# Performance work log

Hardware: AMD Instinct MI355X
Metric: run time of the kernel (lower is better)

## Reference

```python
import jax, jax.numpy as jnp
import numpy as np

B, T, N, H = 16, 12, 1000, 128
NL = 2  # num_layers
EPS = 1e-5


def setup_inputs() -> dict:
    key = jax.random.key(0)
    ks = jax.random.split(key, 16)
    rn = lambda k, s, sc=0.05: jax.random.normal(k, s, jnp.float32) * sc
    return {
        "inputs": jax.random.normal(ks[0], (B, T, N), jnp.float32),
        "adj": jax.random.uniform(ks[1], (N, N), dtype=jnp.float32),
        # per-layer graph-conv params (stacked over NL layers)
        "gc1_w": rn(ks[2], (NL, H + 1, 2 * H)),
        "gc1_b": jnp.ones((NL, 2 * H), jnp.float32),   # bias=1.0 in torch init
        "gc2_w": rn(ks[3], (NL, H + 1, H)),
        "gc2_b": jnp.zeros((NL, H), jnp.float32),
        "ln_g": jnp.ones((NL, H), jnp.float32),
        "ln_b": jnp.zeros((NL, H), jnp.float32),
        "res_w": rn(ks[4], (H,)),   # Linear(1,H) weight squeezed
        "res_b": rn(ks[5], (H,)),
        # GRU tail (unidirectional, 1 layer)
        "gru_wih": rn(ks[6], (3 * H, H)),
        "gru_whh": rn(ks[7], (3 * H, H)),
        "gru_bih": rn(ks[8], (3 * H,)),
        "gru_bhh": rn(ks[9], (3 * H,)),
        "proj_w": rn(ks[10], (H, H)),
        "proj_b": rn(ks[11], (H,)),
        # output MLP
        "out_w1": rn(ks[12], (256, H)),
        "out_b1": rn(ks[13], (256,)),
        "out_w2": rn(ks[14], (H, 256)),
        "out_b2": rn(ks[15], (H,)),
    }


def _laplacian(adj):
    a = jax.nn.softmax(adj, axis=-1)
    m = a + jnp.eye(N, dtype=adj.dtype)           # A + I
    d = m.sum(axis=1)
    dis = jnp.where(d > 0, d ** -0.5, 0.0)
    # matrix.matmul(D^-1/2).T.matmul(D^-1/2)
    return (m * dis[None, :]).T * dis[None, :]


def _gconv(L, x, h, w, b):
    # x: [B,N], h: [B,N,H], concat: [B,N,H+1]
    concat = jnp.concatenate([x[..., None], h], axis=2)
    ac = jnp.einsum("mn,bnk->bmk", L, concat)     # Laplacian graph conv
    return ac @ w + b                              # [B,N,out_dim]


def _cell(L, x, h, w1, b1, w2, b2):
    gates = jax.nn.sigmoid(_gconv(L, x, h, w1, b1))       # [B,N,2H]
    # torch chunks the FLAT [B, N*2H] tensor: split is across nodes!
    flat = gates.reshape(gates.shape[0], N * 2 * H)
    r = flat[:, : N * H].reshape(-1, N, H)
    u = flat[:, N * H :].reshape(-1, N, H)
    c = jnp.tanh(_gconv(L, x, r * h, w2, b2))
    return u * h + (1.0 - u) * c


def _layernorm(x, g, b):
    mu = x.mean(-1, keepdims=True)
    var = jnp.mean((x - mu) ** 2, axis=-1, keepdims=True)
    return (x - mu) * jax.lax.rsqrt(var + EPS) * g + b


def _gru_last(xs, h0, wih, whh, bih, bhh):
    # xs: [T, BN, H]
    def step(h, x):
        gi = x @ wih.T + bih
        gh = h @ whh.T + bhh
        ir, iz, inn = jnp.split(gi, 3, axis=-1)
        hr, hz, hn = jnp.split(gh, 3, axis=-1)
        r = jax.nn.sigmoid(ir + hr)
        z = jax.nn.sigmoid(iz + hz)
        n = jnp.tanh(inn + r * hn)
        return (1.0 - z) * n + z * h, None
    h_last, _ = jax.lax.scan(step, h0, xs)
    return h_last


def reference(inputs, adj, gc1_w, gc1_b, gc2_w, gc2_b, ln_g, ln_b, res_w, res_b,
              gru_wih, gru_whh, gru_bih, gru_bhh, proj_w, proj_b,
              out_w1, out_b1, out_w2, out_b2):
    L = _laplacian(adj)

    def step(hs, x_t):
        x = x_t
        residual = x_t
        new_hs = []
        out = None
        for i in range(NL):
            h = _cell(L, x, hs[i], gc1_w[i], gc1_b[i], gc2_w[i], gc2_b[i])
            new_hs.append(h)
            res = residual[..., None] * res_w + res_b   # Linear(1,H)
            out = _layernorm(h + res, ln_g[i], ln_b[i])  # dropout = identity (eval)
            x = out.mean(axis=2)
            residual = x
        return tuple(new_hs), out

    h0 = tuple(jnp.zeros((B, N, H), jnp.float32) for _ in range(NL))
    xs = jnp.swapaxes(inputs, 0, 1)                 # [T,B,N]
    _, outs = jax.lax.scan(step, h0, xs)            # [T,B,N,H]

    # GRU tail over time, batched across B*N node-sequences
    rnn_xs = jnp.transpose(outs, (0, 1, 2, 3)).reshape(T, B * N, H)
    h_last = _gru_last(rnn_xs, jnp.zeros((B * N, H), jnp.float32),
                       gru_wih, gru_whh, gru_bih, gru_bhh)
    last = h_last @ proj_w.T + proj_b
    o = last.reshape(B, N, H)
    o = jax.nn.relu(o @ out_w1.T + out_b1) @ out_w2.T + out_b2
    return o
```

## Files before the change

### kernel.cpp

```cpp
#include <hip/hip_runtime.h>
#include <math.h>

#define BB 16
#define TT 12
#define NN 1000
#define HH 128
#define CC 129
#define NROW 16000
#define GR 160
#define KP 1024
#define CP2 160
#define SPS 168

#define BUFSZ 26624
#define OFF_SP   79872
#define OFF_SCAL 101376
#define OFF_SST  103936
#define SMEMB    108032
#define OFF_SO   20480

typedef __attribute__((ext_vector_type(4))) float f32x4;
typedef __attribute__((ext_vector_type(8))) __bf16 bf16x8;

#define MFMA16(A, B, C) __builtin_amdgcn_mfma_f32_16x16x32_bf16((A), (B), (C), 0, 0, 0)

__device__ __forceinline__ float sigmoidf_(float x) { return 1.0f / (1.0f + expf(-x)); }

__global__ void k_softmax(const float* __restrict__ adj, float* __restrict__ a) {
    int i = blockIdx.x;
    int t = threadIdx.x;
    __shared__ float red[256];
    float m = -1e30f;
    for (int j = t; j < NN; j += 256) m = fmaxf(m, adj[i * NN + j]);
    red[t] = m; __syncthreads();
    for (int s = 128; s > 0; s >>= 1) { if (t < s) red[t] = fmaxf(red[t], red[t + s]); __syncthreads(); }
    m = red[0]; __syncthreads();
    float sum = 0.f;
    for (int j = t; j < NN; j += 256) sum += expf(adj[i * NN + j] - m);
    red[t] = sum; __syncthreads();
    for (int s = 128; s > 0; s >>= 1) { if (t < s) red[t] += red[t + s]; __syncthreads(); }
    float inv = 1.0f / red[0];
    for (int j = t; j < NN; j += 256) a[i * NN + j] = expf(adj[i * NN + j] - m) * inv;
}

__global__ __launch_bounds__(256) void k_build_Lt(const float* __restrict__ a, __bf16* __restrict__ Lb) {
    __shared__ float s[64][65];
    int bi = blockIdx.x * 64;
    int bj = blockIdx.y * 64;
    int t = threadIdx.x;
    for (int q = t; q < 64 * 64; q += 256) {
        int r = q >> 6, c = q & 63;
        int jj = bj + r, ii = bi + c;
        s[r][c] = (jj < NN && ii < NN) ? a[jj * NN + ii] : 0.f;
    }
    __syncthreads();
    for (int q = t; q < 64 * 64; q += 256) {
        int r = q >> 6, c = q & 63;
        int ii = bi + r, jj = bj + c;
        if (ii < NN && jj < NN)
            Lb[(size_t)ii * KP + jj] = (__bf16)(0.5f * (s[c][r] + (ii == jj ? 1.0f : 0.0f)));
    }
}

__global__ void k_prep(const float* __restrict__ wih, const float* __restrict__ whh,
                       const float* __restrict__ proj_w, const float* __restrict__ ow1,
                       const float* __restrict__ ow2, const float* __restrict__ gc1_w,
                       const float* __restrict__ gc2_w,
                       __bf16* __restrict__ WihB, __bf16* __restrict__ WhhB,
                       __bf16* __restrict__ projB, __bf16* __restrict__ w1B,
                       __bf16* __restrict__ w2B, __bf16* __restrict__ W1t,
                       __bf16* __restrict__ W2t) {
    int idx = blockIdx.x * 256 + threadIdx.x;
    if (idx < 49152) { WihB[idx] = (__bf16)wih[idx]; return; }
    idx -= 49152;
    if (idx < 49152) { WhhB[idx] = (__bf16)whh[idx]; return; }
    idx -= 49152;
    if (idx < 16384) { projB[idx] = (__bf16)proj_w[idx]; return; }
    idx -= 16384;
    if (idx < 32768) { w1B[idx] = (__bf16)ow1[idx]; return; }
    idx -= 32768;
    if (idx < 32768) { w2B[idx] = (__bf16)ow2[idx]; return; }
    idx -= 32768;
    if (idx < 2 * 256 * CP2) {
        int l = idx / (256 * CP2); int r = idx % (256 * CP2); int o = r / CP2, c = r % CP2;
        W1t[idx] = (c < CC) ? (__bf16)gc1_w[((size_t)l * CC + c) * 256 + o] : (__bf16)0.f;
        return;
    }
    idx -= 2 * 256 * CP2;
    if (idx < 2 * 128 * CP2) {
        int l = idx / (128 * CP2); int r = idx % (128 * CP2); int o = r / CP2, c = r % CP2;
        W2t[idx] = (c < CC) ? (__bf16)gc2_w[((size_t)l * CC + c) * 128 + o] : (__bf16)0.f;
    }
}

__global__ void k_prep_x(const float* __restrict__ inp, __bf16* __restrict__ G0) {
    int idx = blockIdx.x * 256 + threadIdx.x;
    if (idx >= BB * 1024) return;
    int b = idx >> 10, k = idx & 1023;
    G0[(size_t)b * GR * KP + k] = (k < NN) ? (__bf16)inp[(size_t)b * TT * NN + k] : (__bf16)0.f;
}

#define GL16(SRC, DSTOFF)                                                            \
    __builtin_amdgcn_global_load_lds(                                                \
        (const __attribute__((address_space(1))) unsigned int*)(SRC),                \
        (__attribute__((address_space(3))) unsigned int*)(smem + (DSTOFF)), 16, 0, 0)

template<int MODE, int STORE>
__global__ __launch_bounds__(1024) void k_fused(
    const __bf16* __restrict__ Lb, const __bf16* __restrict__ Gf,
    const __bf16* __restrict__ Wt, const float* __restrict__ bias,
    __bf16* __restrict__ GB, float* __restrict__ u, float* __restrict__ h,
    const float* __restrict__ x_in, int xstride,
    const float* __restrict__ res_w, const float* __restrict__ res_b,
    const float* __restrict__ ln_g, const float* __restrict__ ln_b,
    float* __restrict__ x_out, __bf16* __restrict__ Gnext,
    __bf16* __restrict__ GhSelf,
    float* __restrict__ hg, __bf16* __restrict__ Hb,
    const __bf16* __restrict__ WihB, const __bf16* __restrict__ WhhB,
    const float* __restrict__ bih, const float* __restrict__ bhh,
    const float* __restrict__ inp, __bf16* __restrict__ xnextG, int tnext)
{
    __shared__ __align__(16) char smem[SMEMB];
    __bf16* sP   = (__bf16*)(smem + OFF_SP);
    __bf16* sGT  = (__bf16*)smem;
    __bf16* sT   = (__bf16*)smem;
    __bf16* sO   = (__bf16*)(smem + OFF_SO);
    float*  sScal= (float*)(smem + OFF_SCAL);
    float*  sSt  = (float*)(smem + OFF_SST);

    int tid = threadIdx.x;
    int wg = blockIdx.x;
    int b = wg & 15;
    int m0 = (wg >> 4) * 64;
    int wave = tid >> 6, lane = tid & 63;
    int lr = lane & 15, lk = lane >> 4;
    int wm = wave >> 3;
    int wcg = wave & 7;
    int cgbase = (wcg == 0) ? 0 : (wcg + 1) * 16;
    int NC = (wcg == 0) ? 2 : 1;

    if (MODE == 0) {
        if (tid < 256) sScal[tid] = bias[tid];
    } else if (tid < 128) {
        sScal[tid] = bias[tid];
        sScal[128 + tid] = res_w[tid];
        sScal[256 + tid] = res_b[tid];
        sScal[384 + tid] = ln_g[tid];
        sScal[512 + tid] = ln_b[tid];
    }

    size_t srowOff = (size_t)b * GR * KP;
    int rIn = lane >> 3;
    int cswz = ((lane & 7) ^ rIn) * 8;

    int ch0 = (wave < 10) ? (2 * wave) : (wave + 10);
    int ch1 = 2 * wave + 1;
    const __bf16* src0 = (ch0 < 8)
        ? Lb + (size_t)(m0 + ch0 * 8 + rIn) * KP + cswz
        : Gf + srowOff + (size_t)((ch0 - 8) * 8 + rIn) * KP + cswz;
    const __bf16* src1 = (wave < 10)
        ? ((ch1 < 8) ? Lb + (size_t)(m0 + ch1 * 8 + rIn) * KP + cswz
                     : Gf + srowOff + (size_t)((ch1 - 8) * 8 + rIn) * KP + cswz)
        : (const __bf16*)nullptr;

#define STAGE(BUF, IT) {                                                \
    GL16(src0 + (IT) * 64, (BUF) * BUFSZ + ch0 * 1024);                 \
    if (wave < 10) GL16(src1 + (IT) * 64, (BUF) * BUFSZ + ch1 * 1024); }

    f32x4 acc[2][2];
#pragma unroll
    for (int i = 0; i < 2; i++)
#pragma unroll
        for (int j = 0; j < 2; j++) acc[i][j] = (f32x4){0.f, 0.f, 0.f, 0.f};

    STAGE(0, 0);
    STAGE(1, 1);
    int bc = 0;
    for (int it = 0; it < 16; ++it) {
        if (it == 15)       asm volatile("s_waitcnt vmcnt(0)" ::: "memory");
        else if (wave < 10) asm volatile("s_waitcnt vmcnt(2)" ::: "memory");
        else                asm volatile("s_waitcnt vmcnt(1)" ::: "memory");
        __builtin_amdgcn_s_barrier();
        __builtin_amdgcn_sched_barrier(0);
        const char* bp = smem + bc * BUFSZ;
#pragma unroll
        for (int ks = 0; ks < 2; ks++) {
            int kb = (ks * 64 + lk * 16) ^ ((lr & 7) << 4);
            bf16x8 af[2];
#pragma unroll
            for (int mf = 0; mf < 2; mf++) {
                int chA = wm * 4 + mf * 2 + (lr >> 3);
                af[mf] = *(const bf16x8*)(bp + chA * 1024 + (lr & 7) * 128 + kb);
            }
#pragma unroll
            for (int cf = 0; cf < 2; cf++) {
                if (cf < NC) {
                    int chB = 8 + (cgbase >> 3) + cf * 2 + (lr >> 3);
                    bf16x8 bfr = *(const bf16x8*)(bp + chB * 1024 + (lr & 7) * 128 + kb);
                    acc[0][cf] = MFMA16(af[0], bfr, acc[0][cf]);
                    acc[1][cf] = MFMA16(af[1], bfr, acc[1][cf]);
                }
            }
        }
        if (it < 14) { int bs = (it + 2) % 3; STAGE(bs, it + 2); }
        bc = (bc == 2) ? 0 : bc + 1;
    }
    __syncthreads();
#undef STAGE

#pragma unroll
    for (int mf = 0; mf < 2; mf++)
#pragma unroll
        for (int cf = 0; cf < 2; cf++) {
            if (cf < NC) {
#pragma unroll
                for (int i = 0; i < 4; i++)
                    sP[(wm * 32 + mf * 16 + lk * 4 + i) * SPS + cgbase + cf * 16 + lr] =
                        (__bf16)acc[mf][cf][i];
            }
        }
    for (int q = tid; q < 64 * 16; q += 1024) sP[(q >> 4) * SPS + 144 + (q & 15)] = (__bf16)0.f;
    __syncthreads();

    constexpr int NOF = (MODE == 0) ? 2 : 1;
    int o0 = wave * NOF * 16;
    f32x4 accs[4][NOF];
#pragma unroll
    for (int i = 0; i < 4; i++)
#pragma unroll
        for (int j = 0; j < NOF; j++) accs[i][j] = (f32x4){0.f, 0.f, 0.f, 0.f};
    if (wave < 8) {
#pragma unroll
        for (int kk2 = 0; kk2 < CP2; kk2 += 32) {
            bf16x8 pa[4];
#pragma unroll
            for (int mf2 = 0; mf2 < 4; mf2++)
                pa[mf2] = *(const bf16x8*)&sP[(mf2 * 16 + lr) * SPS + kk2 + lk * 8];
#pragma unroll
            for (int of = 0; of < NOF; of++) {
                bf16x8 wb = *(const bf16x8*)&Wt[(size_t)(o0 + of * 16 + lr) * CP2 + kk2 + lk * 8];
#pragma unroll
                for (int mf2 = 0; mf2 < 4; mf2++)
                    accs[mf2][of] = MFMA16(pa[mf2], wb, accs[mf2][of]);
            }
        }
    }

    if (MODE == 0) {
        if (tid < 8)
            *(bf16x8*)&GB[srowOff + m0 + tid * 8] = *(const bf16x8*)&Gf[srowOff + m0 + tid * 8];
        bool clean = (m0 + 64 <= 500);
        if (clean) {
            if (wave < 8) {
#pragma unroll
                for (int mf2 = 0; mf2 < 4; mf2++)
#pragma unroll
                    for (int of = 0; of < NOF; of++) {
                        int o = o0 + of * 16 + lr;
                        float bv = sScal[o];
#pragma unroll
                        for (int i = 0; i < 4; i++)
                            sGT[o * 72 + mf2 * 16 + lk * 4 + i] = (__bf16)sigmoidf_(accs[mf2][of][i] + bv);
                    }
            }
            __syncthreads();
            for (int q = tid; q < 128 * 16; q += 1024) {
                int j = q >> 4;
                int rnc = (q & 15) * 4;
                size_t gidx = srowOff + (size_t)(1 + j) * KP + 2 * m0 + rnc * 2;
                bf16x8 hv = *(const bf16x8*)&Gf[gidx];
                bf16x8 rv;
#pragma unroll
                for (int e = 0; e < 8; e++) {
                    int rnl = rnc + (e >> 1);
                    int hi = e & 1;
                    float g = (float)sGT[(hi * 128 + j) * 72 + rnl];
                    rv[e] = (__bf16)(g * (float)hv[e]);
                }
                *(bf16x8*)&GB[gidx] = rv;
            }
        } else if (wave < 8) {
#pragma unroll
            for (int mf2 = 0; mf2 < 4; mf2++)
#pragma unroll
                for (int of = 0; of < NOF; of++) {
                    int o = o0 + of * 16 + lr;
                    int j = o & 127, hi = o >> 7;
                    float bv = sScal[o];
#pragma unroll
                    for (int i = 0; i < 4; i++) {
                        int m = m0 + mf2 * 16 + lk * 4 + i;
                        if (m >= NN) continue;
                        float g = sigmoidf_(accs[mf2][of][i] + bv);
                        if (m < 500) {
                            size_t gi = srowOff + (size_t)(1 + j) * KP + 2 * m + hi;
                            GB[gi] = (__bf16)(g * (float)Gf[gi]);
                        } else {
                            u[((size_t)b * NN + 2 * (m - 500) + hi) * HH + j] = g;
                        }
                    }
                }
        }
    } else {
        int j = o0 + lr;
        float hnv[4][4];
        float mu_[4][4], rs_[4][4];
        float xs_[4][4];
        if (wave < 8) {
            float s_[4][4], ss_[4][4];
#pragma unroll
            for (int a = 0; a < 4; a++)
#pragma unroll
                for (int i = 0; i < 4; i++) { s_[a][i] = 0.f; ss_[a][i] = 0.f; }
            float b2v = sScal[j], rwv = sScal[128 + j], rbv = sScal[256 + j];
#pragma unroll
            for (int mf2 = 0; mf2 < 4; mf2++) {
#pragma unroll
                for (int i = 0; i < 4; i++) {
                    int m = m0 + mf2 * 16 + lk * 4 + i;
                    int msafe = (m < NN) ? m : (NN - 1);
                    size_t ri = ((size_t)b * NN + msafe) * HH + j;
                    float cv = tanhf(accs[mf2][0][i] + b2v);
                    float uu = u[ri];
                    float hv = h[ri];
                    float hn = uu * hv + (1.f - uu) * cv;
                    if (m < NN) h[ri] = hn;
                    hnv[mf2][i] = hn;
                    float xv = (m < NN) ? x_in[(size_t)b * xstride + m] : 0.f;
                    float y = hn + xv * rwv + rbv;
                    accs[mf2][0][i] = y;
                    s_[mf2][i] += y; ss_[mf2][i] += y * y;
                }
            }
#pragma unroll
            for (int msk = 1; msk < 16; msk <<= 1)
#pragma unroll
                for (int a = 0; a < 4; a++)
#pragma unroll
                    for (int i = 0; i < 4; i++) {
                        s_[a][i] += __shfl_xor(s_[a][i], msk);
                        ss_[a][i] += __shfl_xor(ss_[a][i], msk);
                    }
            if (lr == 0) {
#pragma unroll
                for (int a = 0; a < 4; a++)
#pragma unroll
                    for (int i = 0; i < 4; i++) {
                        int ml = a * 16 + lk * 4 + i;
                        sSt[wave * 64 + ml] = s_[a][i];
                        sSt[512 + wave * 64 + ml] = ss_[a][i];
                    }
            }
        }
        __syncthreads();
        if (wave < 8) {
#pragma unroll
            for (int a = 0; a < 4; a++)
#pragma unroll
                for (int i = 0; i < 4; i++) {
                    int ml = a * 16 + lk * 4 + i;
                    float S = 0.f, SS = 0.f;
#pragma unroll
                    for (int w = 0; w < 8; w++) { S += sSt[w * 64 + ml]; SS += sSt[512 + w * 64 + ml]; }
                    float mu = S * (1.f / 128.f);
                    float var = SS * (1.f / 128.f) - mu * mu;
                    mu_[a][i] = mu;
                    rs_[a][i] = rsqrtf(var + 1e-5f);
                }
            float lg = sScal[384 + j], lb2 = sScal[512 + j];
#pragma unroll
            for (int mf2 = 0; mf2 < 4; mf2++)
#pragma unroll
                for (int i = 0; i < 4; i++) {
                    float ov = (accs[mf2][0][i] - mu_[mf2][i]) * rs_[mf2][i] * lg + lb2;
                    accs[mf2][0][i] = ov;
                    xs_[mf2][i] = ov;
                }
#pragma unroll
            for (int msk = 1; msk < 16; msk <<= 1)
#pragma unroll
                for (int a = 0; a < 4; a++)
#pragma unroll
                    for (int i = 0; i < 4; i++) xs_[a][i] += __shfl_xor(xs_[a][i], msk);
        }
        __syncthreads();
        if (wave < 8 && lr == 0) {
#pragma unroll
            for (int a = 0; a < 4; a++)
#pragma unroll
                for (int i = 0; i < 4; i++)
                    sSt[wave * 64 + a * 16 + lk * 4 + i] = xs_[a][i];
        }
        __syncthreads();
        if (wave == 0 && lr == 0) {
#pragma unroll
            for (int a = 0; a < 4; a++)
#pragma unroll
                for (int i = 0; i < 4; i++) {
                    int ml = a * 16 + lk * 4 + i;
                    int m = m0 + ml;
                    if (m < NN) {
                        float S = 0.f;
#pragma unroll
                        for (int w = 0; w < 8; w++) S += sSt[w * 64 + ml];
                        float xv = S * (1.f / 128.f);
                        if (x_out) x_out[(size_t)b * NN + m] = xv;
                        if (Gnext) Gnext[(size_t)b * GR * KP + m] = (__bf16)xv;
                    }
                }
        }
        if (wave < 8) {
#pragma unroll
            for (int mf2 = 0; mf2 < 4; mf2++)
#pragma unroll
                for (int i = 0; i < 4; i++)
                    sT[j * 72 + mf2 * 16 + lk * 4 + i] = (__bf16)hnv[mf2][i];
            if (STORE) {
#pragma unroll
                for (int mf2 = 0; mf2 < 4; mf2++)
#pragma unroll
                    for (int i = 0; i < 4; i++)
                        sO[(mf2 * 16 + lk * 4 + i) * 136 + j] = (__bf16)accs[mf2][0][i];
            }
        }
        __syncthreads();
        for (int q = tid; q < 128 * 8; q += 1024) {
            int jj = q >> 3, mc = (q & 7) * 8;
            if (m0 + mc < NN)
                *(bf16x8*)&GhSelf[srowOff + (size_t)(1 + jj) * KP + m0 + mc] =
                    *(const bf16x8*)&sT[jj * 72 + mc];
        }
        if (STORE) {
            if (wave < 8) {
                float br  = bih[j] + bhh[j];
                float bz  = bih[128 + j] + bhh[128 + j];
                float bni = bih[256 + j], bnh = bhh[256 + j];
                const __bf16* wir = WihB + (size_t)j * HH;
                const __bf16* whr = WhhB + (size_t)j * HH;
                const __bf16* wiz = WihB + (size_t)(128 + j) * HH;
                const __bf16* whz = WhhB + (size_t)(128 + j) * HH;
                const __bf16* win = WihB + (size_t)(256 + j) * HH;
                const __bf16* whn = WhhB + (size_t)(256 + j) * HH;
#pragma unroll
                for (int mf = 0; mf < 4; mf++) {
                    f32x4 gr = (f32x4){0.f,0.f,0.f,0.f}, gz = gr, gni = gr, gnh = gr;
                    int rrow = m0 + mf * 16 + lr;
                    size_t hrow = (size_t)b * NN + ((rrow < NN) ? rrow : (NN - 1));
#pragma unroll
                    for (int kk = 0; kk < 128; kk += 32) {
                        bf16x8 xa = *(const bf16x8*)&sO[(mf * 16 + lr) * 136 + kk + lk * 8];
                        bf16x8 ha = *(const bf16x8*)&Hb[hrow * HH + kk + lk * 8];
                        gr  = MFMA16(xa, *(const bf16x8*)(wir + kk + lk * 8), gr);
                        gr  = MFMA16(ha, *(const bf16x8*)(whr + kk + lk * 8), gr);
                        gz  = MFMA16(xa, *(const bf16x8*)(wiz + kk + lk * 8), gz);
                        gz  = MFMA16(ha, *(const bf16x8*)(whz + kk + lk * 8), gz);
                        gni = MFMA16(xa, *(const bf16x8*)(win + kk + lk * 8), gni);
                        gnh = MFMA16(ha, *(const bf16x8*)(whn + kk + lk * 8), gnh);
                    }
#pragma unroll
                    for (int i = 0; i < 4; i++) {
                        int m = m0 + mf * 16 + lk * 4 + i;
                        if (m >= NN) continue;
                        size_t ri = ((size_t)b * NN + m) * HH + j;
                        float hv = hg[ri];
                        float rg = sigmoidf_(gr[i] + br);
                        float zg = sigmoidf_(gz[i] + bz);
                        float ng = tanhf(gni[i] + bni + rg * (gnh[i] + bnh));
                        float hp = (1.f - zg) * ng + zg * hv;
                        hg[ri] = hp;
                        Hb[ri] = (__bf16)hp;
                    }
                }
            }
            if (tid < 64 && tnext < TT) {
                int n = m0 + tid;
                if (n < NN)
                    xnextG[srowOff + n] = (__bf16)inp[(size_t)b * TT * NN + tnext * NN + n];
            }
        }
    }
}
#undef GL16

__global__ __launch_bounds__(256) void k_head_mfma(const __bf16* __restrict__ Hb,
                                                   const __bf16* __restrict__ projB,
                                                   const float* __restrict__ pb,
                                                   const __bf16* __restrict__ w1B,
                                                   const float* __restrict__ b1,
                                                   const __bf16* __restrict__ w2B,
                                                   const float* __restrict__ b2,
                                                   float* __restrict__ out) {
    __shared__ __align__(16) __bf16 sH1[64 * 136];
    __shared__ __align__(16) __bf16 sH2[64 * 264];
    int tid = threadIdx.x;
    int r0 = blockIdx.x * 64;
    int wv = tid >> 6, lane = tid & 63;
    int lr = lane & 15, lk = lane >> 4;
    int arow = r0 + wv * 16 + lr;

    f32x4 a1[8];
#pragma unroll
    for (int i = 0; i < 8; i++) a1[i] = (f32x4){0.f, 0.f, 0.f, 0.f};
#pragma unroll
    for (int kk = 0; kk < 128; kk += 32) {
        bf16x8 xa = *(const bf16x8*)&Hb[(size_t)arow * HH + kk + lk * 8];
#pragma unroll
        for (int f = 0; f < 8; f++) {
            bf16x8 wb = *(const bf16x8*)&projB[(size_t)(f * 16 + lr) * HH + kk + lk * 8];
            a1[f] = MFMA16(xa, wb, a1[f]);
        }
    }
#pragma unroll
    for (int f = 0; f < 8; f++) {
        int j = f * 16 + lr;
        float bv = pb[j];
#pragma unroll
        for (int i = 0; i < 4; i++)
            sH1[(wv * 16 + lk * 4 + i) * 136 + j] = (__bf16)(a1[f][i] + bv);
    }
    __syncthreads();

    f32x4 a2[16];
#pragma unroll
    for (int i = 0; i < 16; i++) a2[i] = (f32x4){0.f, 0.f, 0.f, 0.f};
#pragma unroll
    for (int kk = 0; kk < 128; kk += 32) {
        bf16x8 pa = *(const bf16x8*)&sH1[(wv * 16 + lr) * 136 + kk + lk * 8];
#pragma unroll
        for (int f = 0; f < 16; f++) {
            bf16x8 wb = *(const bf16x8*)&w1B[(size_t)(f * 16 + lr) * HH + kk + lk * 8];
            a2[f] = MFMA16(pa, wb, a2[f]);
        }
    }
    __syncthreads();
#pragma unroll
    for (int f = 0; f < 16; f++) {
        int o = f * 16 + lr;
        float bv = b1[o];
#pragma unroll
        for (int i = 0; i < 4; i++)
            sH2[(wv * 16 + lk * 4 + i) * 264 + o] = (__bf16)fmaxf(a2[f][i] + bv, 0.f);
    }
    __syncthreads();

    f32x4 a3[8];
#pragma unroll
    for (int i = 0; i < 8; i++) a3[i] = (f32x4){0.f, 0.f, 0.f, 0.f};
#pragma unroll
    for (int kk = 0; kk < 256; kk += 32) {
        bf16x8 pa = *(const bf16x8*)&sH2[(wv * 16 + lr) * 264 + kk + lk * 8];
#pragma unroll
        for (int f = 0; f < 8; f++) {
            bf16x8 wb = *(const bf16x8*)&w2B[(size_t)(f * 16 + lr) * 256 + kk + lk * 8];
            a3[f] = MFMA16(pa, wb, a3[f]);
        }
    }
#pragma unroll
    for (int f = 0; f < 8; f++) {
        int j = f * 16 + lr;
        float bv = b2[j];
#pragma unroll
        for (int i = 0; i < 4; i++)
            out[(size_t)(r0 + wv * 16 + lk * 4 + i) * HH + j] = a3[f][i] + bv;
    }
}

extern "C" void kernel_launch(void* const* d_in, const int* in_sizes, int n_in,
                              void* d_out, int out_size, void* d_ws, size_t ws_size,
                              hipStream_t stream) {
    const float* inp    = (const float*)d_in[0];
    const float* adj    = (const float*)d_in[1];
    const float* gc1_w  = (const float*)d_in[2];
    const float* gc1_b  = (const float*)d_in[3];
    const float* gc2_w  = (const float*)d_in[4];
    const float* gc2_b  = (const float*)d_in[5];
    const float* ln_g   = (const float*)d_in[6];
    const float* ln_b   = (const float*)d_in[7];
    const float* res_w  = (const float*)d_in[8];
    const float* res_b  = (const float*)d_in[9];
    const float* wih    = (const float*)d_in[10];
    const float* whh    = (const float*)d_in[11];
    const float* bih    = (const float*)d_in[12];
    const float* bhh    = (const float*)d_in[13];
    const float* proj_w = (const float*)d_in[14];
    const float* proj_b = (const float*)d_in[15];
    const float* ow1    = (const float*)d_in[16];
    const float* ob1    = (const float*)d_in[17];
    const float* ow2    = (const float*)d_in[18];
    const float* ob2    = (const float*)d_in[19];
    float* out = (float*)d_out;

    char* ws = (char*)d_ws;
    size_t off = 0;
    __bf16* Lb     = (__bf16*)(ws + off); off += (size_t)KP * KP * 2;
    __bf16* Gfull0 = (__bf16*)(ws + off); off += (size_t)BB * GR * KP * 2;
    __bf16* Gfull1 = (__bf16*)(ws + off); off += (size_t)BB * GR * KP * 2;
    __bf16* GfullB = (__bf16*)(ws + off); off += (size_t)BB * GR * KP * 2;
    size_t zgrp1 = off;
    float* h0   = (float*)(ws + off);  off += (size_t)NROW * HH * 4;
    float* h1   = (float*)(ws + off);  off += (size_t)NROW * HH * 4;
    float* hg   = (float*)(ws + off);  off += (size_t)NROW * HH * 4;
    __bf16* Hb  = (__bf16*)(ws + off); off += (size_t)NROW * HH * 2;
    float* u    = (float*)(ws + off);  off += (size_t)NROW * HH * 4;
    float* xB   = (float*)(ws + off);  off += NROW * 4;
    __bf16* W1t = (__bf16*)(ws + off); off += (size_t)2 * 256 * CP2 * 2;
    __bf16* W2t = (__bf16*)(ws + off); off += (size_t)2 * 128 * CP2 * 2;
    __bf16* WihB= (__bf16*)(ws + off); off += 49152 * 2;
    __bf16* WhhB= (__bf16*)(ws + off); off += 49152 * 2;
    __bf16* projB=(__bf16*)(ws + off); off += 16384 * 2;
    __bf16* w1B = (__bf16*)(ws + off); off += 32768 * 2;
    __bf16* w2B = (__bf16*)(ws + off); off += 32768 * 2;
    float* a_sm = u;

    hipMemsetAsync(Lb, 0, zgrp1, stream);
    hipMemsetAsync(h0, 0, (size_t)NROW * HH * 8, stream);
    hipMemsetAsync(hg, 0, (size_t)NROW * HH * 6, stream);

    k_softmax<<<NN, 256, 0, stream>>>(adj, a_sm);
    k_build_Lt<<<dim3(16, 16), 256, 0, stream>>>(a_sm, Lb);
    k_prep<<<1184, 256, 0, stream>>>(wih, whh, proj_w, ow1, ow2, gc1_w, gc2_w,
                                     WihB, WhhB, projB, w1B, w2B, W1t, W2t);
    k_prep_x<<<64, 256, 0, stream>>>(inp, Gfull0);

    for (int t = 0; t < TT; t++) {
        const float* xs0 = inp + (size_t)t * NN;
        k_fused<0, 0><<<256, 1024, 0, stream>>>(Lb, Gfull0, W1t, gc1_b, GfullB, u,
            nullptr, nullptr, 0, nullptr, nullptr, nullptr, nullptr,
            nullptr, nullptr, nullptr,
            nullptr, nullptr, nullptr, nullptr, nullptr, nullptr, nullptr, nullptr, 0);
        k_fused<1, 0><<<256, 1024, 0, stream>>>(Lb, GfullB, W2t, gc2_b, nullptr, u, h0,
            xs0, TT * NN, res_w, res_b, ln_g, ln_b,
            xB, Gfull1, Gfull0,
            nullptr, nullptr, nullptr, nullptr, nullptr, nullptr, nullptr, nullptr, 0);
        k_fused<0, 0><<<256, 1024, 0, stream>>>(Lb, Gfull1, W1t + 256 * CP2, gc1_b + 256, GfullB, u,
            nullptr, nullptr, 0, nullptr, nullptr, nullptr, nullptr,
            nullptr, nullptr, nullptr,
            nullptr, nullptr, nullptr, nullptr, nullptr, nullptr, nullptr, nullptr, 0);
        k_fused<1, 1><<<256, 1024, 0, stream>>>(Lb, GfullB, W2t + 128 * CP2, gc2_b + 128, nullptr, u, h1,
            xB, NN, res_w, res_b, ln_g + 128, ln_b + 128,
            nullptr, nullptr, Gfull1,
            hg, Hb, WihB, WhhB, bih, bhh, inp, Gfull0, t + 1);
    }
    k_head_mfma<<<250, 256, 0, stream>>>(Hb, projB, proj_b, w1B, ob1, w2B, ob2, out);
}
```

Before: 1.444 ms.

## Shrink LDS to double buffering and stage GRU hidden state in shared memory

Replaces the three-stage cp.async-style ring with a two-buffer pipeline and aliases sP onto the staging area, cutting shared memory per block roughly in half so that two 1024-thread blocks may fit per CU. It also adds a launch-bounds occupancy hint. The GRU hidden-state rows are now loaded cooperatively into LDS once instead of being read from global memory by each wave. The price is shallower prefetch, with a full vmcnt(0) wait and barrier every iteration, which can expose load latency. There are also extra syncs to protect the aliased buffers.

After: 2.090 ms. +44.7%, slower.

```diff
diff --git a/kernel.cpp b/kernel.cpp
--- a/kernel.cpp
+++ b/kernel.cpp
@@ -12,12 +12,12 @@
 #define CP2 160
 #define SPS 168
 
-#define BUFSZ 26624
-#define OFF_SP   79872
-#define OFF_SCAL 101376
-#define OFF_SST  103936
-#define SMEMB    108032
-#define OFF_SO   20480
+#define BUFSZ    26624
+#define OFF_SO   18432
+#define OFF_SHB  35840
+#define OFF_SCAL 53248
+#define OFF_SST  55808
+#define SMEMB    59904
 
 typedef __attribute__((ext_vector_type(4))) float f32x4;
 typedef __attribute__((ext_vector_type(8))) __bf16 bf16x8;
@@ -106,7 +106,7 @@
         (__attribute__((address_space(3))) unsigned int*)(smem + (DSTOFF)), 16, 0, 0)
 
 template<int MODE, int STORE>
-__global__ __launch_bounds__(1024) void k_fused(
+__global__ __launch_bounds__(1024, 8) void k_fused(
     const __bf16* __restrict__ Lb, const __bf16* __restrict__ Gf,
     const __bf16* __restrict__ Wt, const float* __restrict__ bias,
     __bf16* __restrict__ GB, float* __restrict__ u, float* __restrict__ h,
@@ -121,7 +121,7 @@
     const float* __restrict__ inp, __bf16* __restrict__ xnextG, int tnext)
 {
     __shared__ __align__(16) char smem[SMEMB];
-    __bf16* sP   = (__bf16*)(smem + OFF_SP);
+    __bf16* sP   = (__bf16*)smem;
     __bf16* sGT  = (__bf16*)smem;
     __bf16* sT   = (__bf16*)smem;
     __bf16* sO   = (__bf16*)(smem + OFF_SO);
@@ -174,14 +174,10 @@
         for (int j = 0; j < 2; j++) acc[i][j] = (f32x4){0.f, 0.f, 0.f, 0.f};
 
     STAGE(0, 0);
-    STAGE(1, 1);
+    __syncthreads();
     int bc = 0;
     for (int it = 0; it < 16; ++it) {
-        if (it == 15)       asm volatile("s_waitcnt vmcnt(0)" ::: "memory");
-        else if (wave < 10) asm volatile("s_waitcnt vmcnt(2)" ::: "memory");
-        else                asm volatile("s_waitcnt vmcnt(1)" ::: "memory");
-        __builtin_amdgcn_s_barrier();
-        __builtin_amdgcn_sched_barrier(0);
+        if (it < 15) STAGE(bc ^ 1, it + 1);
         const char* bp = smem + bc * BUFSZ;
 #pragma unroll
         for (int ks = 0; ks < 2; ks++) {
@@ -202,8 +198,12 @@
                 }
             }
         }
-        if (it < 14) { int bs = (it + 2) % 3; STAGE(bs, it + 2); }
-        bc = (bc == 2) ? 0 : bc + 1;
+        if (it < 15) {
+            asm volatile("s_waitcnt vmcnt(0)" ::: "memory");
+            __builtin_amdgcn_s_barrier();
+            __builtin_amdgcn_sched_barrier(0);
+        }
+        bc ^= 1;
     }
     __syncthreads();
 #undef STAGE
@@ -251,6 +251,7 @@
             *(bf16x8*)&GB[srowOff + m0 + tid * 8] = *(const bf16x8*)&Gf[srowOff + m0 + tid * 8];
         bool clean = (m0 + 64 <= 500);
         if (clean) {
+            __syncthreads();
             if (wave < 8) {
 #pragma unroll
                 for (int mf2 = 0; mf2 < 4; mf2++)
@@ -423,6 +424,15 @@
                         sO[(mf2 * 16 + lk * 4 + i) * 136 + j] = (__bf16)accs[mf2][0][i];
             }
         }
+        if (STORE) {
+            {
+                int row = tid >> 4, c8 = (tid & 15) * 8;
+                int m = m0 + row;
+                size_t hrow = (size_t)b * NN + ((m < NN) ? m : (NN - 1));
+                *(bf16x8*)(smem + OFF_SHB + (row * 136 + c8) * 2) =
+                    *(const bf16x8*)&Hb[hrow * HH + c8];
+            }
+        }
         __syncthreads();
         for (int q = tid; q < 128 * 8; q += 1024) {
             int jj = q >> 3, mc = (q & 7) * 8;
@@ -444,12 +454,10 @@
 #pragma unroll
                 for (int mf = 0; mf < 4; mf++) {
                     f32x4 gr = (f32x4){0.f,0.f,0.f,0.f}, gz = gr, gni = gr, gnh = gr;
-                    int rrow = m0 + mf * 16 + lr;
-                    size_t hrow = (size_t)b * NN + ((rrow < NN) ? rrow : (NN - 1));
 #pragma unroll
                     for (int kk = 0; kk < 128; kk += 32) {
                         bf16x8 xa = *(const bf16x8*)&sO[(mf * 16 + lr) * 136 + kk + lk * 8];
-                        bf16x8 ha = *(const bf16x8*)&Hb[hrow * HH + kk + lk * 8];
+                        bf16x8 ha = *(const bf16x8*)(smem + OFF_SHB + ((mf * 16 + lr) * 136 + kk + lk * 8) * 2);
                         gr  = MFMA16(xa, *(const bf16x8*)(wir + kk + lk * 8), gr);
                         gr  = MFMA16(ha, *(const bf16x8*)(whr + kk + lk * 8), gr);
                         gz  = MFMA16(xa, *(const bf16x8*)(wiz + kk + lk * 8), gz);
```
